# Kernel optimization log

Measured on AMD Instinct MI355X. Metric: run time of the kernel, lower is better.

The kernel has to match this reference:

```python
import jax, jax.numpy as jnp
import numpy as np

B, Q, PAST = 2, 1024, 1024
T = Q + PAST
HID, NH, NKV, HD = 4096, 32, 8, 128
MAXPOS = 4096
SCALE = HD ** -0.5


def setup_inputs() -> dict:
    key = jax.random.key(0)
    ks = jax.random.split(key, 8)
    hidden_states = jax.random.normal(ks[0], (B, Q, HID), jnp.float32)
    attention_mask = jnp.ones((B, T), jnp.int32)  # all tokens valid
    position_ids = jnp.broadcast_to(
        jnp.arange(PAST, PAST + Q, dtype=jnp.int64)[None, :], (B, Q))
    # standard RoPE caches: [max_pos, head_dim/2]
    inv = 1.0 / (10000.0 ** (np.arange(0, HD, 2, dtype=np.float64) / HD))
    ang = np.arange(MAXPOS, dtype=np.float64)[:, None] * inv[None, :]
    rope_cos_freqs = jnp.asarray(np.cos(ang), jnp.float32)
    rope_sin_freqs = jnp.asarray(np.sin(ang), jnp.float32)
    past_key = jax.random.normal(ks[1], (B, NKV, PAST, HD), jnp.float32)
    past_value = jax.random.normal(ks[2], (B, NKV, PAST, HD), jnp.float32)
    q_w = jax.random.normal(ks[3], (NH * HD, HID), jnp.float32) * 0.02
    k_w = jax.random.normal(ks[4], (NKV * HD, HID), jnp.float32) * 0.02
    v_w = jax.random.normal(ks[5], (NKV * HD, HID), jnp.float32) * 0.02
    o_w = jax.random.normal(ks[6], (HID, NH * HD), jnp.float32) * 0.02
    return {"hidden_states": hidden_states, "attention_mask": attention_mask,
            "position_ids": position_ids, "rope_cos_freqs": rope_cos_freqs,
            "rope_sin_freqs": rope_sin_freqs, "past_key": past_key,
            "past_value": past_value, "q_w": q_w, "k_w": k_w, "v_w": v_w,
            "o_w": o_w}


def _rope(x, cos, sin):
    # x: [B,S,n_heads,HD]; cos/sin: [B,S,HD/2]; non-interleaved (half split)
    d2 = x.shape[-1] // 2
    x1, x2 = x[..., :d2], x[..., d2:]
    c, s = cos[:, :, None, :], sin[:, :, None, :]
    return jnp.concatenate([x1 * c - x2 * s, x2 * c + x1 * s], axis=-1)


def reference(hidden_states, attention_mask, position_ids, rope_cos_freqs,
              rope_sin_freqs, past_key, past_value, q_w, k_w, v_w, o_w):
    b, q_len, _ = hidden_states.shape
    q = jnp.einsum('bsh,oh->bso', hidden_states, q_w).reshape(b, q_len, NH, HD)
    k = jnp.einsum('bsh,oh->bso', hidden_states, k_w).reshape(b, q_len, NKV, HD)
    v = jnp.einsum('bsh,oh->bso', hidden_states, v_w).reshape(b, q_len, NKV, HD)

    cos = rope_cos_freqs[position_ids]  # [B,Q,HD/2]
    sin = rope_sin_freqs[position_ids]
    q = _rope(q, cos, sin)
    k = _rope(k, cos, sin)

    # append to KV cache -> [B,NKV,T,HD]
    present_key = jnp.concatenate([past_key, k.transpose(0, 2, 1, 3)], axis=2)
    present_value = jnp.concatenate([past_value, v.transpose(0, 2, 1, 3)], axis=2)

    # additive causal + padding mask built from cumsum of attention_mask
    all_idx = jnp.cumsum(attention_mask, axis=-1)            # [B,T]
    full = (all_idx[:, -q_len:, None] >= all_idx[:, None, :]) \
        & attention_mask[:, None, :].astype(bool)            # [B,Q,T]
    bias = jnp.where(full, 0.0, -10000.0)[:, None, :, :]     # [B,1,Q,T]

    group = NH // NKV
    k_rep = jnp.repeat(present_key, group, axis=1)           # [B,NH,T,HD]
    v_rep = jnp.repeat(present_value, group, axis=1)

    scores = jnp.einsum('bqhd,bhkd->bhqk', q, k_rep) * SCALE + bias
    probs = jax.nn.softmax(scores, axis=-1)
    ctx = jnp.einsum('bhqk,bhkd->bqhd', probs, v_rep).reshape(b, q_len, NH * HD)
    attn_out = jnp.einsum('bso,ho->bsh', ctx, o_w)
    return attn_out, present_key, present_value
```

## Files before the change

### kernel.cpp

```cpp
#include <hip/hip_runtime.h>
#include <hip/hip_bf16.h>
#include <stdint.h>

typedef __bf16 bf16_t;
typedef bf16_t bf16x8 __attribute__((ext_vector_type(8)));
typedef bf16_t bf16x4 __attribute__((ext_vector_type(4)));
typedef float f32x4 __attribute__((ext_vector_type(4)));

#define B_ 2
#define Q_ 1024
#define PAST_ 1024
#define T_ 2048
#define HID_ 4096
#define NH_ 32
#define NKV_ 8
#define HD_ 128
#define SCALE_ 0.08838834764831845f

__device__ __forceinline__ void async_cp16(const bf16_t* g, bf16_t* l) {
  __builtin_amdgcn_global_load_lds((__attribute__((address_space(1))) void*)g,
                                   (__attribute__((address_space(3))) void*)l, 16, 0, 0);
}

__global__ void cvt_f32_bf16(const float* __restrict__ src, bf16_t* __restrict__ dst, size_t n) {
  size_t i = ((size_t)blockIdx.x * blockDim.x + threadIdx.x) * 8;
  if (i >= n) return;
  float4 a = *(const float4*)(src + i);
  float4 b = *(const float4*)(src + i + 4);
  bf16x8 o;
  o[0] = (bf16_t)a.x; o[1] = (bf16_t)a.y; o[2] = (bf16_t)a.z; o[3] = (bf16_t)a.w;
  o[4] = (bf16_t)b.x; o[5] = (bf16_t)b.y; o[6] = (bf16_t)b.z; o[7] = (bf16_t)b.w;
  *(bf16x8*)(dst + i) = o;
}

__global__ void copy_past(const float* __restrict__ pk, const float* __restrict__ pv,
                          float* __restrict__ oK, float* __restrict__ oV,
                          bf16_t* __restrict__ Kall) {
  size_t i = ((size_t)blockIdx.x * 256 + threadIdx.x) * 4;
  if (i >= (size_t)B_ * NKV_ * PAST_ * HD_) return;
  int d = (int)(i & 127);
  size_t r = i >> 7;
  int t = (int)(r & 1023); r >>= 10;
  int g = (int)(r & 7); int b = (int)(r >> 3);
  size_t dst = (((size_t)b * NKV_ + g) * T_ + t) * HD_ + d;
  float4 k4 = *(const float4*)(pk + i);
  float4 v4 = *(const float4*)(pv + i);
  *(float4*)(oK + dst) = k4;
  *(float4*)(oV + dst) = v4;
  bf16x4 kb; kb[0] = (bf16_t)k4.x; kb[1] = (bf16_t)k4.y; kb[2] = (bf16_t)k4.z; kb[3] = (bf16_t)k4.w;
  *(bf16x4*)(Kall + dst) = kb;
}

__global__ void build_vt(const float* __restrict__ past_v, const float* __restrict__ QKV,
                         bf16_t* __restrict__ Vt) {
  __shared__ bf16_t tile[64][136];
  const int tid = threadIdx.x;
  const int t0 = blockIdx.x * 64, g = blockIdx.y, b = blockIdx.z;
#pragma unroll
  for (int k = 0; k < 8; ++k) {
    int idx = k * 256 + tid;
    int t = idx >> 5, dc = (idx & 31) * 4;
    int tt = t0 + t;
    const float* src = (tt < PAST_)
        ? past_v + ((((size_t)b * NKV_ + g) * PAST_ + tt) * HD_ + dc)
        : QKV + (((size_t)b * Q_ + (tt - PAST_)) * 6144 + 5120 + g * HD_ + dc);
    float4 v4 = *(const float4*)src;
    tile[t][dc] = (bf16_t)v4.x; tile[t][dc + 1] = (bf16_t)v4.y;
    tile[t][dc + 2] = (bf16_t)v4.z; tile[t][dc + 3] = (bf16_t)v4.w;
  }
  __syncthreads();
#pragma unroll
  for (int k = 0; k < 4; ++k) {
    int idx = k * 256 + tid;
    int d = idx >> 3, c = idx & 7;
    bf16x8 o;
#pragma unroll
    for (int j = 0; j < 8; ++j) o[j] = tile[c * 8 + j][d];
    *(bf16x8*)(Vt + ((((size_t)b * NKV_ + g) * HD_ + d) * T_) + t0 + c * 8) = o;
  }
}

__device__ __forceinline__ void stage_tile(const bf16_t* __restrict__ G, int ldg,
                                           bf16_t* __restrict__ L, int tid) {
#pragma unroll
  for (int t = 0; t < 4; ++t) {
    int c = t * 512 + tid;
    int row = c >> 3, sc = (c & 7) ^ (row & 7);
    int cb = t * 512 + (tid & 448);
    async_cp16(G + (size_t)row * ldg + sc * 8, L + (size_t)cb * 8);
  }
}

__global__ __launch_bounds__(512, 2)
void gemm256(const bf16_t* __restrict__ A, const bf16_t* __restrict__ W,
             float* __restrict__ C, int M, int N, int K) {
  __shared__ bf16_t sm[2][2][16384];
  const int tid = threadIdx.x;
  const int lane = tid & 63;
  const int quad = lane >> 4, l15 = lane & 15;
  const int wave = tid >> 6;
  const int wm = wave >> 2, wn = wave & 3;
  const int bm = blockIdx.y * 256, bn = blockIdx.x * 256;
  const int NT = K >> 6;

  const bf16_t* Ag = A + (size_t)bm * K;
  const bf16_t* Wg = W + (size_t)bn * K;

  f32x4 acc[8][4] = {};

  stage_tile(Ag, K, &sm[0][0][0], tid);
  stage_tile(Wg, K, &sm[0][1][0], tid);
  stage_tile(Ag + 64, K, &sm[1][0][0], tid);
  stage_tile(Wg + 64, K, &sm[1][1][0], tid);
  asm volatile("s_waitcnt vmcnt(8)" ::: "memory");
  __builtin_amdgcn_s_barrier();

  const int arow = wm * 128 + l15;
  const int brow = wn * 64 + l15;
  const int pq = l15 & 7;

  for (int t = 0; t < NT; ++t) {
    const bf16_t* lA = &sm[t & 1][0][0];
    const bf16_t* lB = &sm[t & 1][1][0];
    const int k2 = (t + 2) << 6;
    bf16x8 af[4][2], bf01[2][2], bf23[2][2];

#pragma unroll
    for (int m = 0; m < 4; ++m)
#pragma unroll
      for (int kk = 0; kk < 2; ++kk)
        af[m][kk] = *(const bf16x8*)(lA + (arow + m * 16) * 64 + ((((kk << 2) + quad) ^ pq) << 3));
#pragma unroll
    for (int n = 0; n < 2; ++n)
#pragma unroll
      for (int kk = 0; kk < 2; ++kk)
        bf01[n][kk] = *(const bf16x8*)(lB + (brow + n * 16) * 64 + ((((kk << 2) + quad) ^ pq) << 3));
    __builtin_amdgcn_s_barrier();
    asm volatile("s_waitcnt lgkmcnt(0)" ::: "memory");
    __builtin_amdgcn_sched_barrier(0);
    __builtin_amdgcn_s_setprio(1);
#pragma unroll
    for (int m = 0; m < 4; ++m)
#pragma unroll
      for (int n = 0; n < 2; ++n)
#pragma unroll
        for (int kk = 0; kk < 2; ++kk)
          acc[m][n] = __builtin_amdgcn_mfma_f32_16x16x32_bf16(af[m][kk], bf01[n][kk], acc[m][n], 0, 0, 0);
    __builtin_amdgcn_s_setprio(0);
    __builtin_amdgcn_s_barrier();

#pragma unroll
    for (int n = 0; n < 2; ++n)
#pragma unroll
      for (int kk = 0; kk < 2; ++kk)
        bf23[n][kk] = *(const bf16x8*)(lB + (brow + (n + 2) * 16) * 64 + ((((kk << 2) + quad) ^ pq) << 3));
    __builtin_amdgcn_s_barrier();
    asm volatile("s_waitcnt lgkmcnt(0)" ::: "memory");
    __builtin_amdgcn_sched_barrier(0);
    __builtin_amdgcn_s_setprio(1);
#pragma unroll
    for (int m = 0; m < 4; ++m)
#pragma unroll
      for (int n = 0; n < 2; ++n)
#pragma unroll
        for (int kk = 0; kk < 2; ++kk)
          acc[m][n + 2] = __builtin_amdgcn_mfma_f32_16x16x32_bf16(af[m][kk], bf23[n][kk], acc[m][n + 2], 0, 0, 0);
    __builtin_amdgcn_s_setprio(0);
    __builtin_amdgcn_s_barrier();

#pragma unroll
    for (int m = 0; m < 4; ++m)
#pragma unroll
      for (int kk = 0; kk < 2; ++kk)
        af[m][kk] = *(const bf16x8*)(lA + (arow + (m + 4) * 16) * 64 + ((((kk << 2) + quad) ^ pq) << 3));
    if (t + 2 < NT) stage_tile(Wg + k2, K, &sm[t & 1][1][0], tid);
    __builtin_amdgcn_s_barrier();
    asm volatile("s_waitcnt lgkmcnt(0)" ::: "memory");
    __builtin_amdgcn_sched_barrier(0);
    __builtin_amdgcn_s_setprio(1);
#pragma unroll
    for (int m = 0; m < 4; ++m)
#pragma unroll
      for (int n = 0; n < 2; ++n)
#pragma unroll
        for (int kk = 0; kk < 2; ++kk)
          acc[m + 4][n + 2] = __builtin_amdgcn_mfma_f32_16x16x32_bf16(af[m][kk], bf23[n][kk], acc[m + 4][n + 2], 0, 0, 0);
    __builtin_amdgcn_s_setprio(0);
    __builtin_amdgcn_s_barrier();

    if (t + 2 < NT) stage_tile(Ag + k2, K, &sm[t & 1][0][0], tid);
    __builtin_amdgcn_s_barrier();
    __builtin_amdgcn_s_setprio(1);
#pragma unroll
    for (int m = 0; m < 4; ++m)
#pragma unroll
      for (int n = 0; n < 2; ++n)
#pragma unroll
        for (int kk = 0; kk < 2; ++kk)
          acc[m + 4][n] = __builtin_amdgcn_mfma_f32_16x16x32_bf16(af[m][kk], bf01[n][kk], acc[m + 4][n], 0, 0, 0);
    __builtin_amdgcn_s_setprio(0);
    if (t + 2 < NT)
      asm volatile("s_waitcnt vmcnt(8)" ::: "memory");
    else if (t + 2 == NT)
      asm volatile("s_waitcnt vmcnt(0)" ::: "memory");
    __builtin_amdgcn_s_barrier();
  }

#pragma unroll
  for (int m = 0; m < 8; ++m) {
    int row0 = bm + wm * 128 + m * 16 + quad * 4;
#pragma unroll
    for (int n = 0; n < 4; ++n) {
      int col = bn + wn * 64 + n * 16 + l15;
#pragma unroll
      for (int r = 0; r < 4; ++r)
        C[(size_t)(row0 + r) * N + col] = acc[m][n][r];
    }
  }
}

__global__ void rope_scatter(const float* __restrict__ QKV, const float* __restrict__ cosf,
                             const float* __restrict__ sinf, const int* __restrict__ pos_ids,
                             bf16_t* __restrict__ Qr, bf16_t* __restrict__ Kall,
                             float* __restrict__ outK, float* __restrict__ outV) {
  int m = blockIdx.x;
  int b = m >> 10, s = m & 1023;
  int pos = pos_ids[(size_t)b * Q_ + s];
  const float* row = QKV + (size_t)m * 6144;
  int tid = threadIdx.x;
  for (int p = tid; p < NH_ * 64; p += 256) {
    int h = p >> 6, d = p & 63;
    float x1 = row[h * 128 + d], x2 = row[h * 128 + d + 64];
    float c = cosf[pos * 64 + d], sn = sinf[pos * 64 + d];
    size_t qb = (((size_t)b * NH_ + h) * Q_ + s) * HD_;
    Qr[qb + d] = (bf16_t)(x1 * c - x2 * sn);
    Qr[qb + d + 64] = (bf16_t)(x2 * c + x1 * sn);
  }
  for (int p = tid; p < NKV_ * 64; p += 256) {
    int g = p >> 6, d = p & 63;
    float x1 = row[4096 + g * 128 + d], x2 = row[4096 + g * 128 + d + 64];
    float c = cosf[pos * 64 + d], sn = sinf[pos * 64 + d];
    float o1 = x1 * c - x2 * sn, o2 = x2 * c + x1 * sn;
    size_t kbi = (((size_t)b * NKV_ + g) * T_ + PAST_ + s) * HD_;
    Kall[kbi + d] = (bf16_t)o1; Kall[kbi + d + 64] = (bf16_t)o2;
    outK[kbi + d] = o1; outK[kbi + d + 64] = o2;
  }
  for (int e = tid; e < NKV_ * HD_; e += 256) {
    int g = e >> 7, d = e & 127;
    float v = row[5120 + g * 128 + d];
    outV[(((size_t)b * NKV_ + g) * T_ + PAST_ + s) * HD_ + d] = v;
  }
}

__global__ __launch_bounds__(256, 4)
void attn_fwd(const bf16_t* __restrict__ Qr, const bf16_t* __restrict__ Kall,
              const bf16_t* __restrict__ Vt, bf16_t* __restrict__ Ctx) {
  __shared__ bf16_t lK[64 * 128];
  __shared__ bf16_t lV[128 * 64];
  __shared__ bf16_t lP[4 * 16 * 64];
  const int tid = threadIdx.x;
  const int wave = tid >> 6, lane = tid & 63;
  const int quad = lane >> 4, l15 = lane & 15;
  const int i = blockIdx.x;
  const int xcd = i & 7;
  const int j = i >> 3;
  const int pairsel = j & 1;
  const int idx = j >> 1;
  const int h_in = idx & 3;
  const int qt = 15 - (idx >> 2);
  const int b = pairsel, kv = xcd;
  const int h = kv * 4 + h_in;
  const int qbase = qt * 64;
  const int wq = qbase + wave * 16;
  const size_t kvbase = ((size_t)b * NKV_ + kv) * T_ * HD_;
  const size_t vtbase = ((size_t)b * NKV_ + kv) * HD_ * T_;
  bf16x8 qf[4];
  {
    const bf16_t* qg = Qr + ((((size_t)b * NH_ + h) * Q_) + wq + l15) * HD_ + quad * 8;
#pragma unroll
    for (int kk = 0; kk < 4; ++kk) qf[kk] = *(const bf16x8*)(qg + kk * 32);
  }
  f32x4 ctx[8] = {};
  float Mr[4], Lr[4];
#pragma unroll
  for (int r = 0; r < 4; ++r) { Mr[r] = -3.0e30f; Lr[r] = 0.0f; }
  bf16_t* lPw = lP + wave * 16 * 64;
  const int kend = PAST_ + qbase + 64;
  const int wlimit = PAST_ + wq + 15;
  for (int kb = 0; kb < kend; kb += 64) {
    __syncthreads();
#pragma unroll
    for (int t = 0; t < 4; ++t) {
      int cb = t * 256 + wave * 64;
      int c = cb + lane;
      int row = c >> 4, sc = (c & 15) ^ (row & 15);
      async_cp16(Kall + kvbase + (size_t)(kb + row) * HD_ + sc * 8, lK + (size_t)cb * 8);
    }
#pragma unroll
    for (int t = 0; t < 4; ++t) {
      int cb = t * 256 + wave * 64;
      int c = cb + lane;
      int d = c >> 3, sc = (c & 7) ^ (d & 7);
      async_cp16(Vt + vtbase + (size_t)d * T_ + kb + sc * 8, lV + (size_t)cb * 8);
    }
    __syncthreads();
    if (kb <= wlimit) {
      f32x4 sacc[4];
#pragma unroll
      for (int nc = 0; nc < 4; ++nc) sacc[nc] = (f32x4){0.f, 0.f, 0.f, 0.f};
#pragma unroll
      for (int nc = 0; nc < 4; ++nc)
#pragma unroll
        for (int kk = 0; kk < 4; ++kk) {
          bf16x8 bk = *(const bf16x8*)(lK + (nc * 16 + l15) * 128 + (((kk * 4 + quad) ^ l15) << 3));
          sacc[nc] = __builtin_amdgcn_mfma_f32_16x16x32_bf16(qf[kk], bk, sacc[nc], 0, 0, 0);
        }
      bool fullvis = (kb + 63 <= PAST_ + wq);
#pragma unroll
      for (int nc = 0; nc < 4; ++nc) {
        int tkey = kb + nc * 16 + l15;
#pragma unroll
        for (int r = 0; r < 4; ++r) {
          float val = sacc[nc][r] * SCALE_;
          if (!fullvis && tkey > PAST_ + wq + quad * 4 + r) val -= 10000.0f;
          sacc[nc][r] = val;
        }
      }
      float alpha[4], rs[4] = {};
#pragma unroll
      for (int r = 0; r < 4; ++r) {
        float tm = fmaxf(fmaxf(sacc[0][r], sacc[1][r]), fmaxf(sacc[2][r], sacc[3][r]));
#pragma unroll
        for (int mmk = 1; mmk < 16; mmk <<= 1) tm = fmaxf(tm, __shfl_xor(tm, mmk, 64));
        float nm = fmaxf(Mr[r], tm);
        alpha[r] = __expf(Mr[r] - nm);
        Mr[r] = nm;
      }
#pragma unroll
      for (int nc = 0; nc < 4; ++nc)
#pragma unroll
        for (int r = 0; r < 4; ++r) {
          float p = __expf(sacc[nc][r] - Mr[r]);
          rs[r] += p;
          int rho = quad * 4 + r;
          int cslot = ((nc * 2 + (l15 >> 3)) ^ (rho & 7));
          lPw[rho * 64 + cslot * 8 + (l15 & 7)] = (bf16_t)p;
        }
#pragma unroll
      for (int r = 0; r < 4; ++r) {
        float s = rs[r];
#pragma unroll
        for (int mmk = 1; mmk < 16; mmk <<= 1) s += __shfl_xor(s, mmk, 64);
        Lr[r] = Lr[r] * alpha[r] + s;
      }
#pragma unroll
      for (int nc2 = 0; nc2 < 8; ++nc2)
#pragma unroll
        for (int r = 0; r < 4; ++r) ctx[nc2][r] *= alpha[r];
      asm volatile("s_waitcnt lgkmcnt(0)" ::: "memory");
#pragma unroll
      for (int kk2 = 0; kk2 < 2; ++kk2) {
        bf16x8 ap = *(const bf16x8*)(lPw + l15 * 64 + (((kk2 * 4 + quad) ^ (l15 & 7)) << 3));
#pragma unroll
        for (int nc2 = 0; nc2 < 8; ++nc2) {
          bf16x8 bv = *(const bf16x8*)(lV + (nc2 * 16 + l15) * 64 + (((kk2 * 4 + quad) ^ (l15 & 7)) << 3));
          ctx[nc2] = __builtin_amdgcn_mfma_f32_16x16x32_bf16(ap, bv, ctx[nc2], 0, 0, 0);
        }
      }
    }
  }
  float inv[4];
#pragma unroll
  for (int r = 0; r < 4; ++r) inv[r] = 1.0f / Lr[r];
#pragma unroll
  for (int nc2 = 0; nc2 < 8; ++nc2)
#pragma unroll
    for (int r = 0; r < 4; ++r) {
      size_t row = (size_t)b * Q_ + wq + quad * 4 + r;
      Ctx[row * (NH_ * HD_) + h * HD_ + nc2 * 16 + l15] = (bf16_t)(ctx[nc2][r] * inv[r]);
    }
}

extern "C" void kernel_launch(void* const* d_in, const int* in_sizes, int n_in,
                              void* d_out, int out_size, void* d_ws, size_t ws_size,
                              hipStream_t stream) {
  const float* hidden = (const float*)d_in[0];
  const int* pos = (const int*)d_in[2];
  const float* cosf = (const float*)d_in[3];
  const float* sinf = (const float*)d_in[4];
  const float* past_k = (const float*)d_in[5];
  const float* past_v = (const float*)d_in[6];
  const float* q_w = (const float*)d_in[7];
  const float* k_w = (const float*)d_in[8];
  const float* v_w = (const float*)d_in[9];
  const float* o_w = (const float*)d_in[10];

  float* attn_out = (float*)d_out;
  float* outK = attn_out + (size_t)B_ * Q_ * HID_;
  float* outV = outK + (size_t)B_ * NKV_ * T_ * HD_;

  if (ws_size < 150994944) return;
  char* ws = (char*)d_ws;
  bf16_t* Wqkv = (bf16_t*)(ws);
  bf16_t* Xb   = (bf16_t*)(ws + 50331648);
  float*  QKV  = (float*)(ws + 67108864);
  bf16_t* Qr   = (bf16_t*)(ws + 117440512);
  bf16_t* Kall = (bf16_t*)(ws + 134217728);
  bf16_t* Vt   = (bf16_t*)(ws + 142606336);
  bf16_t* Wo   = (bf16_t*)(ws + 67108864);
  bf16_t* Ctx  = (bf16_t*)(ws + 50331648);

  cvt_f32_bf16<<<4096, 256, 0, stream>>>(hidden, Xb, 8388608);
  cvt_f32_bf16<<<8192, 256, 0, stream>>>(q_w, Wqkv, 16777216);
  cvt_f32_bf16<<<2048, 256, 0, stream>>>(k_w, Wqkv + 16777216, 4194304);
  cvt_f32_bf16<<<2048, 256, 0, stream>>>(v_w, Wqkv + 20971520, 4194304);
  copy_past<<<2048, 256, 0, stream>>>(past_k, past_v, outK, outV, Kall);
  gemm256<<<dim3(24, 8), 512, 0, stream>>>(Xb, Wqkv, QKV, 2048, 6144, 4096);
  rope_scatter<<<2048, 256, 0, stream>>>(QKV, cosf, sinf, pos, Qr, Kall, outK, outV);
  build_vt<<<dim3(32, 8, 2), 256, 0, stream>>>(past_v, QKV, Vt);
  cvt_f32_bf16<<<8192, 256, 0, stream>>>(o_w, Wo, 16777216);
  attn_fwd<<<1024, 256, 0, stream>>>(Qr, Kall, Vt, Ctx);
  gemm256<<<dim3(16, 8), 512, 0, stream>>>(Ctx, Wo, attn_out, 2048, 4096, 4096);
}
```

Baseline: 624.6 us.

## Double-buffer attention KV tiles and use 128-row GEMM for output projection

The attention kernel now double-buffers K and V tiles in LDS, prefetching the next tile while computing the current one, and raises MFMA priority around the matmuls. Its launch bounds drop to 2 blocks per SM because of the larger LDS footprint. A new gemm128 kernel with a 128x256 tile replaces gemm256 for the output projection, doubling the grid to 256 blocks so more compute units are busy. The risks are lower attention occupancy and more A-tile reloads in the smaller GEMM.

```diff
diff --git a/kernel.cpp b/kernel.cpp
--- a/kernel.cpp
+++ b/kernel.cpp
@@ -91,6 +91,17 @@
   }
 }
 
+__device__ __forceinline__ void stage_tileA128(const bf16_t* __restrict__ G, int ldg,
+                                               bf16_t* __restrict__ L, int tid) {
+#pragma unroll
+  for (int t = 0; t < 2; ++t) {
+    int c = t * 512 + tid;
+    int row = c >> 3, sc = (c & 7) ^ (row & 7);
+    int cb = t * 512 + (tid & 448);
+    async_cp16(G + (size_t)row * ldg + sc * 8, L + (size_t)cb * 8);
+  }
+}
+
 __global__ __launch_bounds__(512, 2)
 void gemm256(const bf16_t* __restrict__ A, const bf16_t* __restrict__ W,
              float* __restrict__ C, int M, int N, int K) {
@@ -209,6 +220,135 @@
 #pragma unroll
   for (int m = 0; m < 8; ++m) {
     int row0 = bm + wm * 128 + m * 16 + quad * 4;
+#pragma unroll
+    for (int n = 0; n < 4; ++n) {
+      int col = bn + wn * 64 + n * 16 + l15;
+#pragma unroll
+      for (int r = 0; r < 4; ++r)
+        C[(size_t)(row0 + r) * N + col] = acc[m][n][r];
+    }
+  }
+}
+
+__global__ __launch_bounds__(512, 2)
+void gemm128(const bf16_t* __restrict__ A, const bf16_t* __restrict__ W,
+             float* __restrict__ C, int M, int N, int K) {
+  __shared__ bf16_t smA[2][8192];
+  __shared__ bf16_t smB[2][16384];
+  const int tid = threadIdx.x;
+  const int lane = tid & 63;
+  const int quad = lane >> 4, l15 = lane & 15;
+  const int wave = tid >> 6;
+  const int wm = wave >> 2, wn = wave & 3;
+  const int bm = blockIdx.y * 128, bn = blockIdx.x * 256;
+  const int NT = K >> 6;
+
+  const bf16_t* Ag = A + (size_t)bm * K;
+  const bf16_t* Wg = W + (size_t)bn * K;
+
+  f32x4 acc[4][4] = {};
+
+  stage_tileA128(Ag, K, &smA[0][0], tid);
+  stage_tile(Wg, K, &smB[0][0], tid);
+  stage_tileA128(Ag + 64, K, &smA[1][0], tid);
+  stage_tile(Wg + 64, K, &smB[1][0], tid);
+  asm volatile("s_waitcnt vmcnt(6)" ::: "memory");
+  __builtin_amdgcn_s_barrier();
+
+  const int arow = wm * 64 + l15;
+  const int brow = wn * 64 + l15;
+  const int pq = l15 & 7;
+
+  for (int t = 0; t < NT; ++t) {
+    const bf16_t* lA = &smA[t & 1][0];
+    const bf16_t* lB = &smB[t & 1][0];
+    const int k2 = (t + 2) << 6;
+    bf16x8 af[2][2], bf01[2][2], bf23[2][2];
+
+#pragma unroll
+    for (int m = 0; m < 2; ++m)
+#pragma unroll
+      for (int kk = 0; kk < 2; ++kk)
+        af[m][kk] = *(const bf16x8*)(lA + (arow + m * 16) * 64 + ((((kk << 2) + quad) ^ pq) << 3));
+#pragma unroll
+    for (int n = 0; n < 2; ++n)
+#pragma unroll
+      for (int kk = 0; kk < 2; ++kk)
+        bf01[n][kk] = *(const bf16x8*)(lB + (brow + n * 16) * 64 + ((((kk << 2) + quad) ^ pq) << 3));
+    __builtin_amdgcn_s_barrier();
+    asm volatile("s_waitcnt lgkmcnt(0)" ::: "memory");
+    __builtin_amdgcn_sched_barrier(0);
+    __builtin_amdgcn_s_setprio(1);
+#pragma unroll
+    for (int m = 0; m < 2; ++m)
+#pragma unroll
+      for (int n = 0; n < 2; ++n)
+#pragma unroll
+        for (int kk = 0; kk < 2; ++kk)
+          acc[m][n] = __builtin_amdgcn_mfma_f32_16x16x32_bf16(af[m][kk], bf01[n][kk], acc[m][n], 0, 0, 0);
+    __builtin_amdgcn_s_setprio(0);
+    __builtin_amdgcn_s_barrier();
+
+#pragma unroll
+    for (int n = 0; n < 2; ++n)
+#pragma unroll
+      for (int kk = 0; kk < 2; ++kk)
+        bf23[n][kk] = *(const bf16x8*)(lB + (brow + (n + 2) * 16) * 64 + ((((kk << 2) + quad) ^ pq) << 3));
+    __builtin_amdgcn_s_barrier();
+    asm volatile("s_waitcnt lgkmcnt(0)" ::: "memory");
+    __builtin_amdgcn_sched_barrier(0);
+    __builtin_amdgcn_s_setprio(1);
+#pragma unroll
+    for (int m = 0; m < 2; ++m)
+#pragma unroll
+      for (int n = 0; n < 2; ++n)
+#pragma unroll
+        for (int kk = 0; kk < 2; ++kk)
+          acc[m][n + 2] = __builtin_amdgcn_mfma_f32_16x16x32_bf16(af[m][kk], bf23[n][kk], acc[m][n + 2], 0, 0, 0);
+    __builtin_amdgcn_s_setprio(0);
+    __builtin_amdgcn_s_barrier();
+
+#pragma unroll
+    for (int m = 0; m < 2; ++m)
+#pragma unroll
+      for (int kk = 0; kk < 2; ++kk)
+        af[m][kk] = *(const bf16x8*)(lA + (arow + (m + 2) * 16) * 64 + ((((kk << 2) + quad) ^ pq) << 3));
+    if (t + 2 < NT) stage_tile(Wg + k2, K, &smB[t & 1][0], tid);
+    __builtin_amdgcn_s_barrier();
+    asm volatile("s_waitcnt lgkmcnt(0)" ::: "memory");
+    __builtin_amdgcn_sched_barrier(0);
+    __builtin_amdgcn_s_setprio(1);
+#pragma unroll
+    for (int m = 0; m < 2; ++m)
+#pragma unroll
+      for (int n = 0; n < 2; ++n)
+#pragma unroll
+        for (int kk = 0; kk < 2; ++kk)
+          acc[m + 2][n + 2] = __builtin_amdgcn_mfma_f32_16x16x32_bf16(af[m][kk], bf23[n][kk], acc[m + 2][n + 2], 0, 0, 0);
+    __builtin_amdgcn_s_setprio(0);
+    __builtin_amdgcn_s_barrier();
+
+    if (t + 2 < NT) stage_tileA128(Ag + k2, K, &smA[t & 1][0], tid);
+    __builtin_amdgcn_s_barrier();
+    __builtin_amdgcn_s_setprio(1);
+#pragma unroll
+    for (int m = 0; m < 2; ++m)
+#pragma unroll
+      for (int n = 0; n < 2; ++n)
+#pragma unroll
+        for (int kk = 0; kk < 2; ++kk)
+          acc[m + 2][n] = __builtin_amdgcn_mfma_f32_16x16x32_bf16(af[m][kk], bf01[n][kk], acc[m + 2][n], 0, 0, 0);
+    __builtin_amdgcn_s_setprio(0);
+    if (t + 2 < NT)
+      asm volatile("s_waitcnt vmcnt(6)" ::: "memory");
+    else if (t + 2 == NT)
+      asm volatile("s_waitcnt vmcnt(0)" ::: "memory");
+    __builtin_amdgcn_s_barrier();
+  }
+
+#pragma unroll
+  for (int m = 0; m < 4; ++m) {
+    int row0 = bm + wm * 64 + m * 16 + quad * 4;
 #pragma unroll
     for (int n = 0; n < 4; ++n) {
       int col = bn + wn * 64 + n * 16 + l15;
@@ -252,11 +392,11 @@
   }
 }
 
-__global__ __launch_bounds__(256, 4)
+__global__ __launch_bounds__(256, 2)
 void attn_fwd(const bf16_t* __restrict__ Qr, const bf16_t* __restrict__ Kall,
               const bf16_t* __restrict__ Vt, bf16_t* __restrict__ Ctx) {
-  __shared__ bf16_t lK[64 * 128];
-  __shared__ bf16_t lV[128 * 64];
+  __shared__ bf16_t lK[2][64 * 128];
+  __shared__ bf16_t lV[2][128 * 64];
   __shared__ bf16_t lP[4 * 16 * 64];
   const int tid = threadIdx.x;
   const int wave = tid >> 6, lane = tid & 63;
@@ -274,47 +414,66 @@
   const int wq = qbase + wave * 16;
   const size_t kvbase = ((size_t)b * NKV_ + kv) * T_ * HD_;
   const size_t vtbase = ((size_t)b * NKV_ + kv) * HD_ * T_;
-  bf16x8 qf[4];
-  {
-    const bf16_t* qg = Qr + ((((size_t)b * NH_ + h) * Q_) + wq + l15) * HD_ + quad * 8;
-#pragma unroll
-    for (int kk = 0; kk < 4; ++kk) qf[kk] = *(const bf16x8*)(qg + kk * 32);
-  }
-  f32x4 ctx[8] = {};
-  float Mr[4], Lr[4];
-#pragma unroll
-  for (int r = 0; r < 4; ++r) { Mr[r] = -3.0e30f; Lr[r] = 0.0f; }
-  bf16_t* lPw = lP + wave * 16 * 64;
-  const int kend = PAST_ + qbase + 64;
-  const int wlimit = PAST_ + wq + 15;
-  for (int kb = 0; kb < kend; kb += 64) {
-    __syncthreads();
+
+  auto stageKV = [&](int kb, int s) {
 #pragma unroll
     for (int t = 0; t < 4; ++t) {
       int cb = t * 256 + wave * 64;
       int c = cb + lane;
       int row = c >> 4, sc = (c & 15) ^ (row & 15);
-      async_cp16(Kall + kvbase + (size_t)(kb + row) * HD_ + sc * 8, lK + (size_t)cb * 8);
+      async_cp16(Kall + kvbase + (size_t)(kb + row) * HD_ + sc * 8, lK[s] + (size_t)cb * 8);
     }
 #pragma unroll
     for (int t = 0; t < 4; ++t) {
       int cb = t * 256 + wave * 64;
       int c = cb + lane;
       int d = c >> 3, sc = (c & 7) ^ (d & 7);
-      async_cp16(Vt + vtbase + (size_t)d * T_ + kb + sc * 8, lV + (size_t)cb * 8);
-    }
-    __syncthreads();
+      async_cp16(Vt + vtbase + (size_t)d * T_ + kb + sc * 8, lV[s] + (size_t)cb * 8);
+    }
+  };
+
+  bf16x8 qf[4];
+  {
+    const bf16_t* qg = Qr + ((((size_t)b * NH_ + h) * Q_) + wq + l15) * HD_ + quad * 8;
+#pragma unroll
+    for (int kk = 0; kk < 4; ++kk) qf[kk] = *(const bf16x8*)(qg + kk * 32);
+  }
+  f32x4 ctx[8] = {};
+  float Mr[4], Lr[4];
+#pragma unroll
+  for (int r = 0; r < 4; ++r) { Mr[r] = -3.0e30f; Lr[r] = 0.0f; }
+  bf16_t* lPw = lP + wave * 16 * 64;
+  const int nt = (PAST_ + qbase + 64) >> 6;
+  const int wlimit = PAST_ + wq + 15;
+
+  stageKV(0, 0);
+
+  for (int ti = 0; ti < nt; ++ti) {
+    const int kb = ti << 6;
+    const int cur = ti & 1;
+    if (ti + 1 < nt) {
+      stageKV(kb + 64, cur ^ 1);
+      asm volatile("s_waitcnt vmcnt(8)" ::: "memory");
+    } else {
+      asm volatile("s_waitcnt vmcnt(0)" ::: "memory");
+    }
+    __builtin_amdgcn_s_barrier();
+    asm volatile("" ::: "memory");
     if (kb <= wlimit) {
+      const bf16_t* cK = lK[cur];
+      const bf16_t* cV = lV[cur];
       f32x4 sacc[4];
 #pragma unroll
       for (int nc = 0; nc < 4; ++nc) sacc[nc] = (f32x4){0.f, 0.f, 0.f, 0.f};
+      __builtin_amdgcn_s_setprio(1);
 #pragma unroll
       for (int nc = 0; nc < 4; ++nc)
 #pragma unroll
         for (int kk = 0; kk < 4; ++kk) {
-          bf16x8 bk = *(const bf16x8*)(lK + (nc * 16 + l15) * 128 + (((kk * 4 + quad) ^ l15) << 3));
+          bf16x8 bk = *(const bf16x8*)(cK + (nc * 16 + l15) * 128 + (((kk * 4 + quad) ^ l15) << 3));
           sacc[nc] = __builtin_amdgcn_mfma_f32_16x16x32_bf16(qf[kk], bk, sacc[nc], 0, 0, 0);
         }
+      __builtin_amdgcn_s_setprio(0);
       bool fullvis = (kb + 63 <= PAST_ + wq);
 #pragma unroll
       for (int nc = 0; nc < 4; ++nc) {
@@ -358,16 +517,21 @@
 #pragma unroll
         for (int r = 0; r < 4; ++r) ctx[nc2][r] *= alpha[r];
       asm volatile("s_waitcnt lgkmcnt(0)" ::: "memory");
+      __builtin_amdgcn_sched_barrier(0);
+      __builtin_amdgcn_s_setprio(1);
 #pragma unroll
       for (int kk2 = 0; kk2 < 2; ++kk2) {
         bf16x8 ap = *(const bf16x8*)(lPw + l15 * 64 + (((kk2 * 4 + quad) ^ (l15 & 7)) << 3));
 #pragma unroll
         for (int nc2 = 0; nc2 < 8; ++nc2) {
-          bf16x8 bv = *(const bf16x8*)(lV + (nc2 * 16 + l15) * 64 + (((kk2 * 4 + quad) ^ (l15 & 7)) << 3));
+          bf16x8 bv = *(const bf16x8*)(cV + (nc2 * 16 + l15) * 64 + (((kk2 * 4 + quad) ^ (l15 & 7)) << 3));
           ctx[nc2] = __builtin_amdgcn_mfma_f32_16x16x32_bf16(ap, bv, ctx[nc2], 0, 0, 0);
         }
       }
-    }
+      __builtin_amdgcn_s_setprio(0);
+    }
+    __builtin_amdgcn_sched_barrier(0);
+    __builtin_amdgcn_s_barrier();
   }
   float inv[4];
 #pragma unroll
@@ -420,5 +584,5 @@
   build_vt<<<dim3(32, 8, 2), 256, 0, stream>>>(past_v, QKV, Vt);
   cvt_f32_bf16<<<8192, 256, 0, stream>>>(o_w, Wo, 16777216);
   attn_fwd<<<1024, 256, 0, stream>>>(Qr, Kall, Vt, Ctx);
-  gemm256<<<dim3(16, 8), 512, 0, stream>>>(Ctx, Wo, attn_out, 2048, 4096, 4096);
-}
+  gemm128<<<dim3(16, 16), 512, 0, stream>>>(Ctx, Wo, attn_out, 2048, 4096, 4096);
+}
```

Result: faster. 581.2 us (-6.9%).
